# Kernel tuning notes

Hardware: AMD Instinct MI355X
Metric: run time of the kernel (lower is better)

## Reference

```python
import jax, jax.numpy as jnp
import numpy as np


def avg_pool_2x2(x):
    # x: [B, H, W, C] -> [B, H//2, W//2, C], non-overlapping 2x2 mean (Keras AveragePooling2D default)
    B, H, W, C = x.shape
    return x.reshape(B, H // 2, 2, W // 2, 2, C).mean(axis=(2, 4))


def setup_inputs() -> dict:
    key = jax.random.key(0)
    k1, k2, k3, k4, k5 = jax.random.split(key, 5)
    B, H, W, C = 16, 64, 64, 512
    x = jax.random.normal(k1, (B, H, W, C), dtype=jnp.float32)
    Wf = jax.random.normal(k2, (C, C // 8), dtype=jnp.float32) * 0.02
    Wg = jax.random.normal(k3, (C, C // 8), dtype=jnp.float32) * 0.02
    Wh = jax.random.normal(k4, (C, C // 2), dtype=jnp.float32) * 0.02
    Wo = jax.random.normal(k5, (C // 2, C), dtype=jnp.float32) * 0.02
    return {"x": x, "Wf": Wf, "Wg": Wg, "Wh": Wh, "Wo": Wo}


def reference(x, Wf, Wg, Wh, Wo):
    B, H, W, C = x.shape
    # 1x1 convs are per-pixel matmuls over channels
    f = jnp.einsum('bhwc,cd->bhwd', x, Wf).reshape(B, H * W, C // 8)          # queries
    xp = avg_pool_2x2(x)                                                      # [B,H/2,W/2,C]
    g = jnp.einsum('bhwc,cd->bhwd', xp, Wg).reshape(B, H * W // 4, C // 8)    # keys
    h = jnp.einsum('bhwc,cd->bhwd', xp, Wh).reshape(B, H * W // 4, C // 2)    # values
    attn = jax.nn.softmax(jnp.einsum('bqd,bkd->bqk', f, g), axis=-1)          # [B, HW, HW/4]
    y = jnp.einsum('bqk,bkd->bqd', attn, h).reshape(B, H, W, C // 2)
    out = jnp.einsum('bhwd,dc->bhwc', y, Wo) + x                              # residual
    return out
```

## Files before the change

### kernel.cpp

```cpp
#include <hip/hip_runtime.h>


#define DEVI static __device__ __forceinline__

typedef float f32x4  __attribute__((ext_vector_type(4)));
typedef float f32x16 __attribute__((ext_vector_type(16)));
typedef short bf16x8 __attribute__((ext_vector_type(8)));

DEVI short f2bf(float f) {
  union { float f; unsigned u; } v; v.f = f;
  unsigned r = v.u + 0x7FFFu + ((v.u >> 16) & 1u);
  return (short)(r >> 16);
}
DEVI float b2f(short s) {
  union { unsigned u; float f; } v; v.u = ((unsigned)(unsigned short)s) << 16; return v.f;
}
DEVI unsigned cvtpk(float lo, float hi) {
  unsigned r;
  asm("v_cvt_pk_bf16_f32 %0, %1, %2" : "=v"(r) : "v"(lo), "v"(hi));
  return r;
}
DEVI f32x4 mfma16(bf16x8 a, bf16x8 b, f32x4 c) {
  return __builtin_amdgcn_mfma_f32_16x16x32_bf16(a, b, c, 0, 0, 0);
}
DEVI f32x16 mfma32(bf16x8 a, bf16x8 b, f32x16 c) {
  return __builtin_amdgcn_mfma_f32_32x32x16_bf16(a, b, c, 0, 0, 0);
}
DEVI void gload16(const short* gsrc, short* lds) {
  __builtin_amdgcn_global_load_lds(
      (const __attribute__((address_space(1))) void*)gsrc,
      (__attribute__((address_space(3))) void*)lds, 16, 0, 0);
}

__global__ __launch_bounds__(256) void prep_weights(
    const float* __restrict__ Wf, const float* __restrict__ Wg,
    const float* __restrict__ Wh, const float* __restrict__ Wo,
    short* __restrict__ WfT, short* __restrict__ WgT,
    short* __restrict__ WhT, short* __restrict__ WoT) {
  int i = blockIdx.x * 256 + threadIdx.x;
  const float* src; short* dst; int K, N, e;
  if (i < 32768)       { src = Wf; dst = WfT; K = 512; N = 64;  e = i; }
  else if (i < 65536)  { src = Wg; dst = WgT; K = 512; N = 64;  e = i - 32768; }
  else if (i < 196608) { src = Wh; dst = WhT; K = 512; N = 256; e = i - 65536; }
  else                 { src = Wo; dst = WoT; K = 256; N = 512; e = i - 196608; }
  int n = e / K, k = e - n * K;
  dst[e] = f2bf(src[(long)k * N + n]);
}

template<bool SRC_F32>
DEVI void stage64(short* lds, const void* gsrc, int rows, int stride, int tid) {
  const int chunks = rows * 8;
  for (int c = tid; c < chunks; c += 256) {
    int row = c >> 3, slot = c & 7;
    int dstb = row*128 + ((slot ^ (row & 7)) << 4);
    if (SRC_F32) {
      const float* s = (const float*)gsrc + (long)row*stride + slot*8;
      float4 u0 = *(const float4*)s;
      float4 u1 = *(const float4*)(s + 4);
      union { unsigned u[4]; bf16x8 v; } pk;
      pk.u[0] = cvtpk(u0.x, u0.y); pk.u[1] = cvtpk(u0.z, u0.w);
      pk.u[2] = cvtpk(u1.x, u1.y); pk.u[3] = cvtpk(u1.z, u1.w);
      *(bf16x8*)((char*)lds + dstb) = pk.v;
    } else {
      *(bf16x8*)((char*)lds + dstb) =
          *(const bf16x8*)((const short*)gsrc + (long)row*stride + slot*8);
    }
  }
}

template<bool A_F32, bool POOL>
__global__ __launch_bounds__(256) void gemm_k512(const void* __restrict__ A,
    const short* __restrict__ BT, short* __restrict__ C, int Nfull,
    short* __restrict__ xp, float cscale) {
  __shared__ short As[128*64];
  __shared__ short Bs[64*64];
  const int m0 = blockIdx.x * 128;
  const int n0 = blockIdx.y * 64;
  const int tid = threadIdx.x, w = tid >> 6, lane = tid & 63;
  const int l15 = lane & 15, lhi = lane >> 4;
  const int wr = w >> 1, wc = w & 1;
  f32x4 acc[4][2] = {};
  for (int kt = 0; kt < 8; ++kt) {
    const int k0 = kt * 64;
    if constexpr (A_F32)
      stage64<true >(As, (const float*)A + (long)m0*512 + k0, 128, 512, tid);
    else
      stage64<false>(As, (const short*)A + (long)m0*512 + k0, 128, 512, tid);
    stage64<false>(Bs, BT + (long)n0*512 + k0, 64, 512, tid);
    __syncthreads();
    if constexpr (POOL) {
      const long pr0 = (long)(m0 >> 12)*1024 + ((m0 & 4095) >> 7)*32;
      int wp = tid >> 3, cs = tid & 7;
      const char* Ab = (const char*)As;
      bf16x8 v00 = *(const bf16x8*)(Ab + (2*wp  )*128 + ((cs ^ ((2*wp  )&7))<<4));
      bf16x8 v01 = *(const bf16x8*)(Ab + (2*wp+1)*128 + ((cs ^ ((2*wp+1)&7))<<4));
      bf16x8 v10 = *(const bf16x8*)(Ab + (64+2*wp)*128 + ((cs ^ ((2*wp  )&7))<<4));
      bf16x8 v11 = *(const bf16x8*)(Ab + (65+2*wp)*128 + ((cs ^ ((2*wp+1)&7))<<4));
      float s[8];
      #pragma unroll
      for (int j = 0; j < 8; ++j)
        s[j] = 0.25f*(b2f(v00[j])+b2f(v01[j])+b2f(v10[j])+b2f(v11[j]));
      union { unsigned u[4]; bf16x8 v; } pk;
      pk.u[0] = cvtpk(s[0], s[1]); pk.u[1] = cvtpk(s[2], s[3]);
      pk.u[2] = cvtpk(s[4], s[5]); pk.u[3] = cvtpk(s[6], s[7]);
      *(bf16x8*)(xp + (pr0 + wp)*512 + k0 + cs*8) = pk.v;
    }
    bf16x8 af[4][2], bfr[2][2];
    #pragma unroll
    for (int mi = 0; mi < 4; ++mi)
      #pragma unroll
      for (int ks = 0; ks < 2; ++ks) {
        int m = wr*64 + mi*16 + l15;
        int slot = lhi + ks*4;
        af[mi][ks] = *(const bf16x8*)((const char*)As + m*128 + ((slot ^ (m & 7)) << 4));
      }
    #pragma unroll
    for (int ni = 0; ni < 2; ++ni)
      #pragma unroll
      for (int ks = 0; ks < 2; ++ks) {
        int n = wc*32 + ni*16 + l15;
        int slot = lhi + ks*4;
        bfr[ni][ks] = *(const bf16x8*)((const char*)Bs + n*128 + ((slot ^ (n & 7)) << 4));
      }
    #pragma unroll
    for (int ks = 0; ks < 2; ++ks)
      #pragma unroll
      for (int mi = 0; mi < 4; ++mi)
        #pragma unroll
        for (int ni = 0; ni < 2; ++ni)
          acc[mi][ni] = mfma16(af[mi][ks], bfr[ni][ks], acc[mi][ni]);
    __syncthreads();
  }
  #pragma unroll
  for (int mi = 0; mi < 4; ++mi)
    #pragma unroll
    for (int ni = 0; ni < 2; ++ni)
      #pragma unroll
      for (int r = 0; r < 4; ++r) {
        long row = m0 + wr*64 + mi*16 + lhi*4 + r;
        int col = n0 + wc*32 + ni*16 + l15;
        C[row * (long)Nfull + col] = f2bf(acc[mi][ni][r] * cscale);
      }
}

__global__ __launch_bounds__(256) void transpose_h(const short* __restrict__ h,
                                                   short* __restrict__ hT) {
  __shared__ short t[64][72];
  const int k0 = blockIdx.x * 64, n0 = blockIdx.y * 64, b = blockIdx.z;
  const int tid = threadIdx.x;
  {
    int row = tid >> 2, cch = (tid & 3) * 16;
    const short* src = h + ((long)b*1024 + k0 + row) * 256 + n0 + cch;
    *(bf16x8*)&t[row][cch]     = *(const bf16x8*)src;
    *(bf16x8*)&t[row][cch + 8] = *(const bf16x8*)(src + 8);
  }
  __syncthreads();
  {
    int n = tid >> 2, kch = (tid & 3) * 16;
    bf16x8 lo, hi;
    #pragma unroll
    for (int j = 0; j < 8; ++j) { lo[j] = t[kch + j][n]; hi[j] = t[kch + 8 + j][n]; }
    short* dst = hT + ((long)b*256 + n0 + n) * 1024 + k0 + kch;
    *(bf16x8*)dst       = lo;
    *(bf16x8*)(dst + 8) = hi;
  }
}

__global__ __launch_bounds__(256, 2) void attn_kernel(const short* __restrict__ f,
    const short* __restrict__ g, const short* __restrict__ hT,
    short* __restrict__ y) {
  extern __shared__ __align__(16) char smem[];
  const int bid = blockIdx.x;
  const int xcd = bid & 7, idx = bid >> 3;
  const int b = xcd*2 + (idx >> 5);
  const int q0 = (idx & 31) * 128;
  const int tid = threadIdx.x, w = tid >> 6, lane = tid & 63;
  const int l31 = lane & 31, hi = lane >> 5;

  bf16x8 fq[4];
  {
    const short* frow = f + ((long)b*4096 + q0 + w*32 + l31) * 64;
    #pragma unroll
    for (int ks = 0; ks < 4; ++ks) fq[ks] = *(const bf16x8*)(frow + ks*16 + hi*8);
  }

  f32x16 acc2[8] = {};
  float rsq = 0.f;

  auto stage = [&](int buf, int kt) {
    const int k0 = kt * 64;
    short* gbuf = (short*)(smem + buf*8192);
    short* hbuf = (short*)(smem + 16384 + buf*32768);
    #pragma unroll
    for (int it = 0; it < 2; ++it) {
      int c = it*256 + w*64 + lane;
      int row = c >> 3, gslot = (c & 7) ^ (row & 7);
      gload16(g + ((long)b*1024 + k0 + row)*64 + gslot*8, gbuf + (it*256 + w*64)*8);
    }
    #pragma unroll
    for (int it = 0; it < 8; ++it) {
      int c = it*256 + w*64 + lane;
      int row = c >> 3, gslot = (c & 7) ^ (row & 7);
      gload16(hT + ((long)b*256 + row)*1024 + k0 + gslot*8, hbuf + (it*256 + w*64)*8);
    }
  };

  stage(0, 0);
  int cur = 0;
  for (int kt = 0; kt < 16; ++kt) {
    if (kt < 15) {
      stage(cur ^ 1, kt + 1);
      asm volatile("s_waitcnt vmcnt(10)" ::: "memory");
    } else {
      asm volatile("s_waitcnt vmcnt(0)" ::: "memory");
    }
    __builtin_amdgcn_s_barrier();
    const char* gcur = (const char*)(smem + cur*8192);
    const char* hcur = (const char*)(smem + 16384 + cur*32768);
    bf16x8 pa[4];
    #pragma unroll
    for (int kc2 = 0; kc2 < 2; ++kc2) {
      f32x16 s2 = {};
      #pragma unroll
      for (int ks = 0; ks < 4; ++ks) {
        int key = kc2*32 + l31;
        bf16x8 gb = *(const bf16x8*)(gcur + key*128 + (((ks*2 + hi) ^ (l31 & 7)) << 4));
        s2 = mfma32(gb, fq[ks], s2);
      }
      #pragma unroll
      for (int fh = 0; fh < 2; ++fh) {
        const int G = fh*8;
        float e0 = exp2f(s2[G+0]), e1 = exp2f(s2[G+1]);
        float e2 = exp2f(s2[G+2]), e3 = exp2f(s2[G+3]);
        float e4 = exp2f(s2[G+4]), e5 = exp2f(s2[G+5]);
        float e6 = exp2f(s2[G+6]), e7 = exp2f(s2[G+7]);
        rsq += ((e0 + e1) + (e2 + e3)) + ((e4 + e5) + (e6 + e7));
        unsigned a0 = cvtpk(e0, e1), a1 = cvtpk(e2, e3);
        unsigned b0 = cvtpk(e4, e5), b1 = cvtpk(e6, e7);
        asm volatile("v_permlane32_swap_b32 %0, %1" : "+v"(b0), "+v"(a0));
        asm volatile("v_permlane32_swap_b32 %0, %1" : "+v"(b1), "+v"(a1));
        union { unsigned u[4]; bf16x8 v; } pk;
        pk.u[0] = a0; pk.u[1] = a1; pk.u[2] = b0; pk.u[3] = b1;
        pa[kc2*2 + fh] = pk.v;
      }
    }
    __builtin_amdgcn_s_setprio(1);
    #pragma unroll
    for (int ks = 0; ks < 4; ++ks) {
      #pragma unroll
      for (int nc2 = 0; nc2 < 8; ++nc2) {
        int n = nc2*32 + l31;
        bf16x8 hb = *(const bf16x8*)(hcur + n*128 + (((ks*2 + hi) ^ (l31 & 7)) << 4));
        acc2[nc2] = mfma32(hb, pa[ks], acc2[nc2]);
      }
    }
    __builtin_amdgcn_s_setprio(0);
    __builtin_amdgcn_s_barrier();
    cur ^= 1;
  }
  rsq += __shfl_xor(rsq, 32);
  float ri = 1.f / rsq;
  short* yw = (short*)(smem + w*16384);
  #pragma unroll
  for (int nc2 = 0; nc2 < 8; ++nc2) {
    #pragma unroll
    for (int fh = 0; fh < 2; ++fh) {
      const int G = fh*8;
      unsigned a0 = cvtpk(acc2[nc2][G+0]*ri, acc2[nc2][G+1]*ri);
      unsigned a1 = cvtpk(acc2[nc2][G+2]*ri, acc2[nc2][G+3]*ri);
      unsigned b0 = cvtpk(acc2[nc2][G+4]*ri, acc2[nc2][G+5]*ri);
      unsigned b1 = cvtpk(acc2[nc2][G+6]*ri, acc2[nc2][G+7]*ri);
      asm volatile("v_permlane32_swap_b32 %0, %1" : "+v"(b0), "+v"(a0));
      asm volatile("v_permlane32_swap_b32 %0, %1" : "+v"(b1), "+v"(a1));
      union { unsigned u[4]; bf16x8 v; } pk;
      pk.u[0] = a0; pk.u[1] = a1; pk.u[2] = b0; pk.u[3] = b1;
      int s = (nc2*2 + fh)*2 + hi;
      *(bf16x8*)(yw + l31*256 + ((s ^ l31) * 8)) = pk.v;
    }
  }
  const long qb = (long)b*4096 + q0 + w*32;
  #pragma unroll
  for (int i = 0; i < 16; ++i) {
    int row = i*2 + hi;
    int s = l31 ^ row;
    bf16x8 v = *(const bf16x8*)(yw + row*256 + l31*8);
    *(bf16x8*)(y + (qb + row)*256 + s*8) = v;
  }
}

__global__ __launch_bounds__(256) void gemm_out(const short* __restrict__ y,
    const short* __restrict__ WoT, const float* __restrict__ x,
    float* __restrict__ out) {
  __shared__ short ys[128*256];
  const int q0 = blockIdx.x * 128;
  const int tid = threadIdx.x, w = tid >> 6, lane = tid & 63;
  const int l31 = lane & 31, hi = lane >> 5;
  #pragma unroll
  for (int it = 0; it < 16; ++it) {
    int c = it*256 + tid;
    int row = c >> 5, gslot = (c & 31) ^ (row & 31);
    gload16(y + ((long)q0 + row)*256 + gslot*8, ys + c*8);
  }
  asm volatile("s_waitcnt vmcnt(0)" ::: "memory");
  __builtin_amdgcn_s_barrier();
  const int qr = w*32 + l31;
  bf16x8 ya[16];
  #pragma unroll
  for (int kk = 0; kk < 16; ++kk) {
    int s = kk*2 + hi;
    ya[kk] = *(const bf16x8*)(ys + qr*256 + ((s ^ (qr & 31)) * 8));
  }
  const long obase = (long)q0 * 512;
  for (int it = 0; it < 16; ++it) {
    const int c0 = it * 32;
    bf16x8 bw[16];
    const short* wrow = WoT + ((long)(c0 + l31))*256 + hi*8;
    #pragma unroll
    for (int ns = 0; ns < 16; ++ns) bw[ns] = *(const bf16x8*)(wrow + ns*16);
    float xv[16];
    #pragma unroll
    for (int r = 0; r < 16; ++r) {
      int rowoff = (r&3) + 8*(r>>2) + 4*hi;
      xv[r] = x[obase + (long)(w*32 + rowoff)*512 + c0 + l31];
    }
    f32x16 ao0 = {}, ao1 = {};
    #pragma unroll
    for (int ns2 = 0; ns2 < 8; ++ns2) {
      ao0 = mfma32(ya[2*ns2  ], bw[2*ns2  ], ao0);
      ao1 = mfma32(ya[2*ns2+1], bw[2*ns2+1], ao1);
    }
    #pragma unroll
    for (int r = 0; r < 16; ++r) {
      int rowoff = (r&3) + 8*(r>>2) + 4*hi;
      out[obase + (long)(w*32 + rowoff)*512 + c0 + l31] = ao0[r] + ao1[r] + xv[r];
    }
  }
}

extern "C" void kernel_launch(void* const* d_in, const int* in_sizes, int n_in,
                              void* d_out, int out_size, void* d_ws, size_t ws_size,
                              hipStream_t stream) {
  const float* x  = (const float*)d_in[0];
  const float* Wf = (const float*)d_in[1];
  const float* Wg = (const float*)d_in[2];
  const float* Wh = (const float*)d_in[3];
  const float* Wo = (const float*)d_in[4];
  float* out = (float*)d_out;

  short* xp  = (short*)d_ws;
  short* fb  = xp  + (long)16*1024*512;
  short* gb  = fb  + (long)65536*64;
  short* hb  = gb  + (long)16384*64;
  short* hTb = hb  + (long)16384*256;
  short* yb  = hTb + (long)16*256*1024;
  short* WfT = yb  + (long)65536*256;
  short* WgT = WfT + 64*512;
  short* WhT = WgT + 64*512;
  short* WoT = WhT + 256*512;

  hipFuncSetAttribute((const void*)attn_kernel,
                      hipFuncAttributeMaxDynamicSharedMemorySize, 81920);

  const float LOG2E = 1.44269504f;
  prep_weights<<<1536, 256, 0, stream>>>(Wf, Wg, Wh, Wo, WfT, WgT, WhT, WoT);
  gemm_k512<true , true ><<<dim3(512, 1), 256, 0, stream>>>((const void*)x,  WfT, fb, 64,  xp, LOG2E);
  gemm_k512<false, false><<<dim3(128, 1), 256, 0, stream>>>((const void*)xp, WgT, gb, 64,  nullptr, 1.0f);
  gemm_k512<false, false><<<dim3(128, 4), 256, 0, stream>>>((const void*)xp, WhT, hb, 256, nullptr, 1.0f);
  transpose_h <<<dim3(16, 4, 16), 256, 0, stream>>>(hb, hTb);
  attn_kernel <<<512, 256, 81920, stream>>>(fb, gb, hTb, yb);
  gemm_out    <<<512, 256, 0, stream>>>(yb, WoT, x, out);
}
```

Baseline: 211.9 us.

## Restructure output GEMM: smaller row tiles, staged residual, double-buffered weights

The output projection kernel now handles 32 query rows per block instead of 128, launching 2048 blocks. Each of the four waves covers a quarter of the 512 output channels rather than a 32-row slice over all channels. The residual x tile is loaded into shared memory with coalesced 16-byte async loads, replacing strided per-element global reads. The Wo fragments are double-buffered in registers so the next channel block's loads overlap the current MFMAs. In exchange, each block requests 80KB of dynamic LDS, which limits occupancy, and weight reuse per block drops.

After: 221.5 us. 1.05x slower.

```diff
diff --git a/kernel.cpp b/kernel.cpp
--- a/kernel.cpp
+++ b/kernel.cpp
@@ -291,48 +291,59 @@
 __global__ __launch_bounds__(256) void gemm_out(const short* __restrict__ y,
     const short* __restrict__ WoT, const float* __restrict__ x,
     float* __restrict__ out) {
-  __shared__ short ys[128*256];
-  const int q0 = blockIdx.x * 128;
+  extern __shared__ __align__(16) char smem[];
+  short* ys = (short*)smem;
+  float* xs = (float*)(smem + 16384);
+  const int q0 = blockIdx.x * 32;
   const int tid = threadIdx.x, w = tid >> 6, lane = tid & 63;
   const int l31 = lane & 31, hi = lane >> 5;
   #pragma unroll
-  for (int it = 0; it < 16; ++it) {
+  for (int it = 0; it < 4; ++it) {
     int c = it*256 + tid;
-    int row = c >> 5, gslot = (c & 31) ^ (row & 31);
+    int row = c >> 5, gslot = (c & 31) ^ row;
     gload16(y + ((long)q0 + row)*256 + gslot*8, ys + c*8);
   }
+  #pragma unroll
+  for (int j = 0; j < 16; ++j) {
+    int c = j*256 + tid;
+    int row = c >> 7, cc = (c & 127) * 4;
+    gload16((const short*)(x + ((long)q0 + row)*512 + cc), (short*)(xs + c*4));
+  }
+  asm volatile("s_waitcnt vmcnt(16)" ::: "memory");
+  __builtin_amdgcn_s_barrier();
+  bf16x8 ya[16];
+  #pragma unroll
+  for (int kk = 0; kk < 16; ++kk)
+    ya[kk] = *(const bf16x8*)(ys + l31*256 + (((kk*2 + hi) ^ l31) * 8));
   asm volatile("s_waitcnt vmcnt(0)" ::: "memory");
   __builtin_amdgcn_s_barrier();
-  const int qr = w*32 + l31;
-  bf16x8 ya[16];
-  #pragma unroll
-  for (int kk = 0; kk < 16; ++kk) {
-    int s = kk*2 + hi;
-    ya[kk] = *(const bf16x8*)(ys + qr*256 + ((s ^ (qr & 31)) * 8));
-  }
-  const long obase = (long)q0 * 512;
-  for (int it = 0; it < 16; ++it) {
-    const int c0 = it * 32;
-    bf16x8 bw[16];
-    const short* wrow = WoT + ((long)(c0 + l31))*256 + hi*8;
-    #pragma unroll
-    for (int ns = 0; ns < 16; ++ns) bw[ns] = *(const bf16x8*)(wrow + ns*16);
-    float xv[16];
+  const int cb = w * 4;
+  bf16x8 wo[2][16];
+  {
+    const short* wrow0 = WoT + ((long)((cb + 0)*32 + l31))*256 + hi*8;
+    #pragma unroll
+    for (int ns = 0; ns < 16; ++ns) wo[0][ns] = *(const bf16x8*)(wrow0 + ns*16);
+  }
+  #pragma unroll
+  for (int it = 0; it < 4; ++it) {
+    const int cur = it & 1, nxt = cur ^ 1;
+    const int c0 = (cb + it) * 32;
+    if (it < 3) {
+      const short* wrown = WoT + ((long)(c0 + 32 + l31))*256 + hi*8;
+      #pragma unroll
+      for (int ns = 0; ns < 16; ++ns) wo[nxt][ns] = *(const bf16x8*)(wrown + ns*16);
+    }
+    f32x16 ao0 = {}, ao1 = {};
+    #pragma unroll
+    for (int ns2 = 0; ns2 < 8; ++ns2) {
+      ao0 = mfma32(ya[2*ns2  ], wo[cur][2*ns2  ], ao0);
+      ao1 = mfma32(ya[2*ns2+1], wo[cur][2*ns2+1], ao1);
+    }
     #pragma unroll
     for (int r = 0; r < 16; ++r) {
       int rowoff = (r&3) + 8*(r>>2) + 4*hi;
-      xv[r] = x[obase + (long)(w*32 + rowoff)*512 + c0 + l31];
-    }
-    f32x16 ao0 = {}, ao1 = {};
-    #pragma unroll
-    for (int ns2 = 0; ns2 < 8; ++ns2) {
-      ao0 = mfma32(ya[2*ns2  ], bw[2*ns2  ], ao0);
-      ao1 = mfma32(ya[2*ns2+1], bw[2*ns2+1], ao1);
-    }
-    #pragma unroll
-    for (int r = 0; r < 16; ++r) {
-      int rowoff = (r&3) + 8*(r>>2) + 4*hi;
-      out[obase + (long)(w*32 + rowoff)*512 + c0 + l31] = ao0[r] + ao1[r] + xv[r];
+      float xv = xs[rowoff*512 + c0 + l31];
+      out[((long)q0 + rowoff)*512 + c0 + l31] = ao0[r] + ao1[r] + xv;
     }
   }
 }
@@ -360,6 +371,8 @@
 
   hipFuncSetAttribute((const void*)attn_kernel,
                       hipFuncAttributeMaxDynamicSharedMemorySize, 81920);
+  hipFuncSetAttribute((const void*)gemm_out,
+                      hipFuncAttributeMaxDynamicSharedMemorySize, 81920);
 
   const float LOG2E = 1.44269504f;
   prep_weights<<<1536, 256, 0, stream>>>(Wf, Wg, Wh, Wo, WfT, WgT, WhT, WoT);
@@ -368,5 +381,5 @@
   gemm_k512<false, false><<<dim3(128, 4), 256, 0, stream>>>((const void*)xp, WhT, hb, 256, nullptr, 1.0f);
   transpose_h <<<dim3(16, 4, 16), 256, 0, stream>>>(hb, hTb);
   attn_kernel <<<512, 256, 81920, stream>>>(fb, gb, hTb, yb);
-  gemm_out    <<<512, 256, 0, stream>>>(yb, WoT, x, out);
-}
+  gemm_out    <<<2048, 256, 81920, stream>>>(yb, WoT, x, out);
+}
```
